# Kernel optimization log

Hardware: AMD Instinct MI355X
Metric: run time of the kernel (lower is better)

## Reference

```python
import jax, jax.numpy as jnp
import numpy as np

B, L, DIM, N, D = 8, 273, 1536, 12, 128
ZS, F_HIS = 256, 32  # image tokens per frame, cache_frame_max
EPS = 1e-6


def rmsnorm(x, g, eps=EPS):
    return x * jax.lax.rsqrt(jnp.mean(x * x, axis=-1, keepdims=True) + eps) * g


def rope_apply(x, freqs):
    # x: [B, T, N, D]; freqs: [T, D//2] angles. Rotate consecutive pairs.
    xp = x.reshape(*x.shape[:-1], D // 2, 2)
    c = jnp.cos(freqs)[None, :, None, :]
    s = jnp.sin(freqs)[None, :, None, :]
    o1 = xp[..., 0] * c - xp[..., 1] * s
    o2 = xp[..., 0] * s + xp[..., 1] * c
    return jnp.stack([o1, o2], axis=-1).reshape(x.shape)


def setup_inputs() -> dict:
    key = jax.random.key(0)
    ks = jax.random.split(key, 10)
    rn = lambda k, shp, sc=1.0: jax.random.normal(k, shp, dtype=jnp.float32) * sc
    return {
        "x": rn(ks[0], (B, L, DIM)),
        "w_q": rn(ks[1], (DIM, DIM), 0.02), "b_q": jnp.zeros((DIM,), jnp.float32),
        "w_k": rn(ks[2], (DIM, DIM), 0.02), "b_k": jnp.zeros((DIM,), jnp.float32),
        "w_v": rn(ks[3], (DIM, DIM), 0.02), "b_v": jnp.zeros((DIM,), jnp.float32),
        "w_o": rn(ks[4], (DIM, DIM), 0.02), "b_o": jnp.zeros((DIM,), jnp.float32),
        "g_q": jnp.ones((DIM,), jnp.float32), "g_k": jnp.ones((DIM,), jnp.float32),
        "cache_k": rn(ks[5], (B, F_HIS * L, N, D)),
        "cache_v": rn(ks[6], (B, F_HIS * L, N, D)),
        "rope_table": jax.random.uniform(ks[7], (64, L, D // 2), dtype=jnp.float32) * (2.0 * np.pi),
        "read_rope_indices": jnp.arange(F_HIS, dtype=jnp.int32),
        "current_frame_idx": 20,
    }


def reference(x, w_q, b_q, w_k, b_k, w_v, b_v, w_o, b_o, g_q, g_k,
              cache_k, cache_v, rope_table, read_rope_indices, current_frame_idx):
    b, s = x.shape[:2]
    f = 1  # one new frame per step (s == L)
    # qkv projections with RMSNorm over full dim (pre head split)
    q = rmsnorm(x @ w_q.T + b_q, g_q).reshape(b, s, N, D)
    k = rmsnorm(x @ w_k.T + b_k, g_k).reshape(b, s, N, D)
    v = (x @ w_v.T + b_v).reshape(b, s, N, D)
    # KV-cache ring-buffer store at slot = frame_idx % cache_frame_max
    slot = current_frame_idx % F_HIS
    cache_k = jax.lax.dynamic_update_slice(cache_k, k, (0, slot * L, 0, 0))
    cache_v = jax.lax.dynamic_update_slice(cache_v, v, (0, slot * L, 0, 0))
    # RoPE angles: history for each cache slot, last for the current frame
    freqs_his = rope_table[read_rope_indices].reshape(F_HIS * L, D // 2)
    freqs_last = rope_table[current_frame_idx]  # [L, D//2]
    q_r = rope_apply(q, freqs_last)
    k_r = rope_apply(cache_k, freqs_his)
    # frame-major views: [b, frames, tokens_per_frame, n, d]
    q_r = q_r.reshape(b, f, L, N, D)
    k_r = k_r.reshape(b, F_HIS, L, N, D)
    v_his = cache_v.reshape(b, F_HIS, L, N, D)
    q_img, k_img, v_img = q_r[:, :, :ZS], k_r[:, :, :ZS], v_his[:, :, :ZS]
    # temporal attention per spatial (image) token, non-causal, masked to valid frames
    scale = 1.0 / jnp.sqrt(jnp.asarray(D, jnp.float32))
    scores = jnp.einsum('bfznd,bgznd->bznfg', q_img, k_img) * scale  # [b,zs,n,f,f_his]
    valid = jnp.minimum(current_frame_idx + 1, F_HIS)
    keep = jnp.arange(F_HIS) < valid
    scores = jnp.where(keep[None, None, None, None, :], scores, -1e30)
    p = jax.nn.softmax(scores, axis=-1)
    x_img = jnp.einsum('bznfg,bgznd->bfznd', p, v_img)  # [b, f, zs, n, d]
    # condition tokens bypass attention: pass through v of the current frame
    v_cond = v.reshape(b, f, L, N, D)[:, :, ZS:]
    out = jnp.concatenate([x_img, v_cond], axis=2).reshape(b, s, N * D)
    return out @ w_o.T + b_o


if __name__ == '__main__':
    o = reference(**setup_inputs())
    print(o.shape)
```

## Files before the change

### kernel.cpp

```cpp
#include <hip/hip_runtime.h>
#include <hip/hip_bf16.h>
#include <stdint.h>

typedef unsigned short u16;
typedef __attribute__((ext_vector_type(8))) short bf16x8;
typedef __attribute__((ext_vector_type(4))) float f32x4;

#define B_    8
#define L_    273
#define DIM_  1536
#define NH_   12
#define DH_   128
#define ZS_   256
#define FH_   32
#define MROWS (B_ * L_)
#define MPAD  2304
#define NQKV  4608
#define WN_   (DIM_ * DIM_)
#define WN8_  (WN_ / 8)
#define X8_   (MROWS * DIM_ / 8)
#define XT8_  (MPAD * DIM_ / 8)

#define N0_ 442368
#define N1_ 737280
#define N2_ 1032192
#define N3_ 1327104
#define N4_ 1622016
#define N5_ 1626624
#define N6_ 2150912
#define PREP_BLKS 8402

#define ATTN_ITEMS (B_ * ZS_ * 6)
#define ATTN_BLKS  (ATTN_ITEMS / 2)
#define VCOND_TOT  (B_ * (L_ - ZS_) * DIM_ / 8)
#define VCOND_BLKS ((VCOND_TOT + 255) / 256)

#define KSPLIT 768

#define OFF_XB    0ULL
#define OFF_WB    7077888ULL
#define OFF_WOB   21233664ULL
#define OFF_BQKV  25952256ULL
#define OFF_CQKV  25970688ULL
#define OFF_ATTN  47204352ULL
#define OFF_SC    54282240ULL
#define OFF_P0    0ULL
#define OFF_P1    25970688ULL

__device__ __forceinline__ u16 f2bf(float f) {
  __hip_bfloat16 h = __float2bfloat16(f);
  return *reinterpret_cast<u16*>(&h);
}
__device__ __forceinline__ float bf2f(u16 v) {
  uint32_t u = ((uint32_t)v) << 16;
  return __uint_as_float(u);
}

__device__ __forceinline__ void gload_lds16(const u16* g, u16* l) {
  __builtin_amdgcn_global_load_lds(
      (const __attribute__((address_space(1))) void*)g,
      (__attribute__((address_space(3))) void*)l,
      16, 0, 0);
}

__device__ __forceinline__ void cast8(const float* __restrict__ s, u16* __restrict__ d,
                                      int i, int nvalid) {
  uint4 o;
  if (i < nvalid) {
    const float4 a = ((const float4*)s)[i * 2];
    const float4 b = ((const float4*)s)[i * 2 + 1];
    o.x = (uint32_t)f2bf(a.x) | ((uint32_t)f2bf(a.y) << 16);
    o.y = (uint32_t)f2bf(a.z) | ((uint32_t)f2bf(a.w) << 16);
    o.z = (uint32_t)f2bf(b.x) | ((uint32_t)f2bf(b.y) << 16);
    o.w = (uint32_t)f2bf(b.z) | ((uint32_t)f2bf(b.w) << 16);
  } else {
    o = make_uint4(0, 0, 0, 0);
  }
  ((uint4*)d)[i] = o;
}

__global__ __launch_bounds__(256)
void prep_kernel(const float* __restrict__ x, const float* __restrict__ w_q,
                 const float* __restrict__ w_k, const float* __restrict__ w_v,
                 const float* __restrict__ w_o, const float* __restrict__ bq,
                 const float* __restrict__ bk, const float* __restrict__ bv,
                 const float* __restrict__ rope_tb, const int* __restrict__ rope_ix,
                 u16* __restrict__ xb, u16* __restrict__ wb, u16* __restrict__ wob,
                 float* __restrict__ bqkv, float* __restrict__ sctab) {
  const int t = blockIdx.x * 256 + threadIdx.x;
  if (t < N0_)      cast8(x,   xb,           t,       X8_);
  else if (t < N1_) cast8(w_q, wb,           t - N0_, WN8_);
  else if (t < N2_) cast8(w_k, wb + WN_,     t - N1_, WN8_);
  else if (t < N3_) cast8(w_v, wb + 2 * WN_, t - N2_, WN8_);
  else if (t < N4_) cast8(w_o, wob,          t - N3_, WN8_);
  else if (t < N5_) {
    int i = t - N4_;
    float v;
    if (i < DIM_)          v = bq[i];
    else if (i < 2 * DIM_) v = bk[i - DIM_];
    else                   v = bv[i - 2 * DIM_];
    bqkv[i] = v;
  } else {
    int u = t - N5_;
    int j = u & 63;
    int idx = u >> 6;
    int f = idx >> 8, z = idx & 255;
    int fi = rope_ix[f];
    float fr = rope_tb[((size_t)fi * L_ + z) * 64 + j];
    float sn, cn;
    __sincosf(fr, &sn, &cn);
    *(float2*)&sctab[((size_t)idx << 7) + 2 * j] = make_float2(sn, cn);
  }
}

__global__ __launch_bounds__(256)
void gemm_bt_kernel(const u16* __restrict__ A, const u16* __restrict__ Bm,
                    const float* __restrict__ bias, void* __restrict__ Cv,
                    void* __restrict__ Cv2,
                    int K, int ldc, int Mvalid, int mode, int ksplit) {
  const int tn = blockIdx.x, tm = blockIdx.y;
  const int tid = threadIdx.x;
  const int lane = tid & 63;
  const int wid = tid >> 6;
  const int wm = wid >> 1, wn = wid & 1;

  __shared__ __align__(16) u16 As[2][128 * 32];
  __shared__ __align__(16) u16 Bs[2][128 * 32];

  f32x4 acc[4][4] = {};

  const int srow = tid >> 2;
  const int scol = (tid & 3) * 8;
  const u16* Abase = A + (size_t)(tm * 128 + srow) * K + scol;
  const u16* Bbase = Bm + (size_t)(tn * 128 + srow) * K + scol;
  const size_t rstep = (size_t)64 * K;
  const int lofs = srow * 32 + scol;

  const int ko = (lane >> 4) * 8;
  const int rA = wm * 64 + (lane & 15);
  const int rB = wn * 64 + (lane & 15);

  const int k0 = blockIdx.z * ksplit;
  const int k1 = k0 + ksplit;

  gload_lds16(Abase + k0,         &As[0][lofs]);
  gload_lds16(Abase + k0 + rstep, &As[0][64 * 32 + lofs]);
  gload_lds16(Bbase + k0,         &Bs[0][lofs]);
  gload_lds16(Bbase + k0 + rstep, &Bs[0][64 * 32 + lofs]);
  __syncthreads();

  int cur = 0;
  for (int kt = k0; kt < k1; kt += 32) {
    const int nx = cur ^ 1;
    if (kt + 32 < k1) {
      gload_lds16(Abase + kt + 32,         &As[nx][lofs]);
      gload_lds16(Abase + kt + 32 + rstep, &As[nx][64 * 32 + lofs]);
      gload_lds16(Bbase + kt + 32,         &Bs[nx][lofs]);
      gload_lds16(Bbase + kt + 32 + rstep, &Bs[nx][64 * 32 + lofs]);
    }
    bf16x8 af[4], bfr[4];
#pragma unroll
    for (int f = 0; f < 4; ++f) {
      af[f]  = *(const bf16x8*)&As[cur][(rA + f * 16) * 32 + ko];
      bfr[f] = *(const bf16x8*)&Bs[cur][(rB + f * 16) * 32 + ko];
    }
#pragma unroll
    for (int fm = 0; fm < 4; ++fm)
#pragma unroll
      for (int fn = 0; fn < 4; ++fn)
        acc[fm][fn] = __builtin_amdgcn_mfma_f32_16x16x32_bf16(af[fm], bfr[fn], acc[fm][fn], 0, 0, 0);
    __syncthreads();
    cur = nx;
  }

  const int m0 = tm * 128 + wm * 64 + (lane >> 4) * 4;
  const int n0 = tn * 128 + wn * 64 + (lane & 15);
  float* Cf = (mode == 2 && blockIdx.z) ? (float*)Cv2 : (float*)Cv;
#pragma unroll
  for (int fm = 0; fm < 4; ++fm) {
#pragma unroll
    for (int fn = 0; fn < 4; ++fn) {
      const int n = n0 + fn * 16;
      const float bv = (mode == 2) ? 0.f : bias[n];
#pragma unroll
      for (int r = 0; r < 4; ++r) {
        const int m = m0 + fm * 16 + r;
        if (m < Mvalid) {
          const float val = acc[fm][fn][r] + bv;
          if (mode == 1) ((u16*)Cv)[(size_t)m * ldc + n] = f2bf(val);
          else           Cf[(size_t)m * ldc + n] = val;
        }
      }
    }
  }
}

__global__ __launch_bounds__(256)
void rmsnorm_rope_kernel(u16* __restrict__ C, const float* __restrict__ g_q,
                         const float* __restrict__ g_k, const float* __restrict__ rope_table,
                         const int* __restrict__ cf_ptr) {
  const int z = blockIdx.x % ZS_;
  const int b = blockIdx.x / ZS_;
  const int m = b * L_ + z;
  const int tid = threadIdx.x;
  const int cf = *cf_ptr;
  u16* row = C + (size_t)m * NQKV;
  __shared__ float red[4];

  for (int sec = 0; sec < 2; ++sec) {
    u16* p = row + sec * DIM_;
    const float* gw = sec ? g_k : g_q;
    float vx[3], vy[3];
    float ss = 0.f;
#pragma unroll
    for (int j = 0; j < 3; ++j) {
      int pj = tid + j * 256;
      uint32_t u = *(const uint32_t*)&p[pj * 2];
      vx[j] = bf2f((u16)(u & 0xffff));
      vy[j] = bf2f((u16)(u >> 16));
      ss += vx[j] * vx[j] + vy[j] * vy[j];
    }
#pragma unroll
    for (int o = 32; o; o >>= 1) ss += __shfl_xor(ss, o);
    if ((tid & 63) == 0) red[tid >> 6] = ss;
    __syncthreads();
    const float tot = red[0] + red[1] + red[2] + red[3];
    const float r = rsqrtf(tot * (1.f / DIM_) + 1e-6f);
#pragma unroll
    for (int j = 0; j < 3; ++j) {
      int pj = tid + j * 256;
      float y0 = vx[j] * r * gw[pj * 2];
      float y1 = vy[j] * r * gw[pj * 2 + 1];
      if (sec == 0) {
        float fr = rope_table[((size_t)cf * L_ + z) * 64 + (pj & 63)];
        float sn, cn;
        __sincosf(fr, &sn, &cn);
        float o0 = y0 * cn - y1 * sn;
        float o1 = y0 * sn + y1 * cn;
        y0 = o0; y1 = o1;
      }
      *(uint32_t*)&p[pj * 2] = (uint32_t)f2bf(y0) | ((uint32_t)f2bf(y1) << 16);
    }
    __syncthreads();
  }
}

__global__ __launch_bounds__(256)
void attention_kernel(const u16* __restrict__ Cq, const float* __restrict__ cache_k,
                      const float* __restrict__ cache_v, const float* __restrict__ sctab,
                      const int* __restrict__ cf_ptr, u16* __restrict__ attn_in) {
  if (blockIdx.x >= ATTN_BLKS) {
    int i = (blockIdx.x - ATTN_BLKS) * 256 + threadIdx.x;
    if (i < VCOND_TOT) {
      int e = i * 8;
      int col = e % DIM_;
      int r = e / DIM_;
      int b = r / (L_ - ZS_);
      int lz = r % (L_ - ZS_);
      size_t mrow = (size_t)b * L_ + ZS_ + lz;
      *(uint4*)&attn_in[mrow * DIM_ + col] = *(const uint4*)&Cq[mrow * NQKV + 2 * DIM_ + col];
    }
    return;
  }

  __shared__ float sm[2][64][6];
  const int p = threadIdx.x >> 7;
  const int wi = (threadIdx.x >> 6) & 1;
  const int lane = threadIdx.x & 63;
  const int item = blockIdx.x * 2 + p;
  const int hp = item % 6;
  const int z = (item / 6) % ZS_;
  const int b = item / (6 * ZS_);
  const int h = lane >> 5, il = lane & 31;
  const int n = hp * 2 + h;
  const int d0 = il * 4;
  const int cf = *cf_ptr;
  const int slot = cf % FH_;
  const int valid = min(cf + 1, FH_);
  const int g0 = (valid + 1) >> 1;
  const int gs = wi ? g0 : 0;
  const int ge = wi ? valid : g0;

  const size_t crow = (size_t)(b * L_ + z) * NQKV + n * DH_ + d0;
  float q0, q1, q2, q3;
  {
    ushort4 qv = *(const ushort4*)&Cq[crow];
    q0 = bf2f(qv.x); q1 = bf2f(qv.y); q2 = bf2f(qv.z); q3 = bf2f(qv.w);
  }

  float mx = -1e30f, lsum = 0.f;
  float a0 = 0.f, a1 = 0.f, a2 = 0.f, a3 = 0.f;
  for (int g = gs; g < ge; ++g) {
    const float4 sc = *(const float4*)&sctab[((size_t)(g * ZS_ + z) << 7) + d0];
    float k0, k1, k2, k3, v0, v1, v2, v3;
    if (g == slot) {
      ushort4 kv = *(const ushort4*)&Cq[crow + DIM_];
      ushort4 vv = *(const ushort4*)&Cq[crow + 2 * DIM_];
      k0 = bf2f(kv.x); k1 = bf2f(kv.y); k2 = bf2f(kv.z); k3 = bf2f(kv.w);
      v0 = bf2f(vv.x); v1 = bf2f(vv.y); v2 = bf2f(vv.z); v3 = bf2f(vv.w);
    } else {
      const size_t coff = ((((size_t)b * FH_ + g) * L_ + z) * NH_ + n) * DH_ + d0;
      const float4 kk = *(const float4*)&cache_k[coff];
      const float4 vv = *(const float4*)&cache_v[coff];
      k0 = kk.x; k1 = kk.y; k2 = kk.z; k3 = kk.w;
      v0 = vv.x; v1 = vv.y; v2 = vv.z; v3 = vv.w;
    }
    const float kr0 = k0 * sc.y - k1 * sc.x;
    const float kr1 = k0 * sc.x + k1 * sc.y;
    const float kr2 = k2 * sc.w - k3 * sc.z;
    const float kr3 = k2 * sc.z + k3 * sc.w;
    float part = q0 * kr0 + q1 * kr1 + q2 * kr2 + q3 * kr3;
#pragma unroll
    for (int o = 16; o; o >>= 1) part += __shfl_xor(part, o);
    const float score = part * 0.088388347648318447f;
    const float nm = fmaxf(mx, score);
    const float scl = __expf(mx - nm);
    const float pw = __expf(score - nm);
    lsum = lsum * scl + pw;
    a0 = a0 * scl + pw * v0;
    a1 = a1 * scl + pw * v1;
    a2 = a2 * scl + pw * v2;
    a3 = a3 * scl + pw * v3;
    mx = nm;
  }

  if (wi == 1) {
    sm[p][lane][0] = mx;  sm[p][lane][1] = lsum;
    sm[p][lane][2] = a0;  sm[p][lane][3] = a1;
    sm[p][lane][4] = a2;  sm[p][lane][5] = a3;
  }
  __syncthreads();
  if (wi == 0) {
    const float mB = sm[p][lane][0], lB = sm[p][lane][1];
    const float M = fmaxf(mx, mB);
    const float wA = __expf(mx - M), wB = __expf(mB - M);
    const float L = lsum * wA + lB * wB;
    const float inv = 1.f / L;
    const float o0 = (a0 * wA + sm[p][lane][2] * wB) * inv;
    const float o1 = (a1 * wA + sm[p][lane][3] * wB) * inv;
    const float o2 = (a2 * wA + sm[p][lane][4] * wB) * inv;
    const float o3 = (a3 * wA + sm[p][lane][5] * wB) * inv;
    uint2 o;
    o.x = (uint32_t)f2bf(o0) | ((uint32_t)f2bf(o1) << 16);
    o.y = (uint32_t)f2bf(o2) | ((uint32_t)f2bf(o3) << 16);
    *(uint2*)&attn_in[(size_t)(b * L_ + z) * DIM_ + n * DH_ + d0] = o;
  }
}

__global__ __launch_bounds__(256)
void reduce_kernel(const float* __restrict__ p0, const float* __restrict__ p1,
                   const float* __restrict__ b_o, float* __restrict__ out) {
  const int i = blockIdx.x * 256 + threadIdx.x;
  if (i >= MROWS * DIM_ / 4) return;
  const int col4 = i % (DIM_ / 4);
  const float4 a = ((const float4*)p0)[i];
  const float4 b = ((const float4*)p1)[i];
  const float4 c = ((const float4*)b_o)[col4];
  float4 o;
  o.x = a.x + b.x + c.x;
  o.y = a.y + b.y + c.y;
  o.z = a.z + b.z + c.z;
  o.w = a.w + b.w + c.w;
  ((float4*)out)[i] = o;
}

extern "C" void kernel_launch(void* const* d_in, const int* in_sizes, int n_in,
                              void* d_out, int out_size, void* d_ws, size_t ws_size,
                              hipStream_t stream) {
  const float* x       = (const float*)d_in[0];
  const float* w_q     = (const float*)d_in[1];
  const float* b_q     = (const float*)d_in[2];
  const float* w_k     = (const float*)d_in[3];
  const float* b_k     = (const float*)d_in[4];
  const float* w_v     = (const float*)d_in[5];
  const float* b_v     = (const float*)d_in[6];
  const float* w_o     = (const float*)d_in[7];
  const float* b_o     = (const float*)d_in[8];
  const float* g_q     = (const float*)d_in[9];
  const float* g_k     = (const float*)d_in[10];
  const float* cache_k = (const float*)d_in[11];
  const float* cache_v = (const float*)d_in[12];
  const float* rope_tb = (const float*)d_in[13];
  const int*   rope_ix = (const int*)d_in[14];
  const int*   cf      = (const int*)d_in[15];

  char* ws = (char*)d_ws;
  u16*   xb      = (u16*)(ws + OFF_XB);
  u16*   wb      = (u16*)(ws + OFF_WB);
  u16*   wob     = (u16*)(ws + OFF_WOB);
  float* bqkv    = (float*)(ws + OFF_BQKV);
  u16*   Cq      = (u16*)(ws + OFF_CQKV);
  u16*   attn_in = (u16*)(ws + OFF_ATTN);
  float* sctab   = (float*)(ws + OFF_SC);
  float* p0      = (float*)(ws + OFF_P0);
  float* p1      = (float*)(ws + OFF_P1);

  prep_kernel<<<PREP_BLKS, 256, 0, stream>>>(x, w_q, w_k, w_v, w_o, b_q, b_k, b_v,
                                             rope_tb, rope_ix, xb, wb, wob, bqkv, sctab);

  gemm_bt_kernel<<<dim3(NQKV / 128, MPAD / 128, 1), 256, 0, stream>>>(
      xb, wb, bqkv, Cq, nullptr, DIM_, NQKV, MPAD, 1, DIM_);

  rmsnorm_rope_kernel<<<B_ * ZS_, 256, 0, stream>>>(Cq, g_q, g_k, rope_tb, cf);

  attention_kernel<<<ATTN_BLKS + VCOND_BLKS, 256, 0, stream>>>(
      Cq, cache_k, cache_v, sctab, cf, attn_in);

  gemm_bt_kernel<<<dim3(DIM_ / 128, MPAD / 128, 2), 256, 0, stream>>>(
      attn_in, wob, nullptr, p0, p1, DIM_, DIM_, MPAD, 2, KSPLIT);

  reduce_kernel<<<(MROWS * DIM_ / 4 + 255) / 256, 256, 0, stream>>>(p0, p1, b_o, (float*)d_out);
}
```

Baseline: 224.0 us.

## Split RMSNorm into stats-only kernel, fuse scaling and q-RoPE into attention; remap GEMM tiles

The in-place RMSNorm+RoPE pass over the QKV buffer becomes a small kernel that only writes per-row inverse RMS values. The gain and query RoPE are applied inside the attention kernel, with the current-frame sin/cos precomputed as an extra row of the prep table. This removes a read-modify-write of the Q and K sections. Separately, the GEMM block index is remapped to interleave tiles across 8 groups, presumably for better cache or XCD locality.

```diff
diff --git a/kernel.cpp b/kernel.cpp
--- a/kernel.cpp
+++ b/kernel.cpp
@@ -27,8 +27,8 @@
 #define N3_ 1327104
 #define N4_ 1622016
 #define N5_ 1626624
-#define N6_ 2150912
-#define PREP_BLKS 8402
+#define N6_ 2167296
+#define PREP_BLKS 8466
 
 #define ATTN_ITEMS (B_ * ZS_ * 6)
 #define ATTN_BLKS  (ATTN_ITEMS / 2)
@@ -44,6 +44,7 @@
 #define OFF_CQKV  25970688ULL
 #define OFF_ATTN  47204352ULL
 #define OFF_SC    54282240ULL
+#define OFF_RMS   58607616ULL
 #define OFF_P0    0ULL
 #define OFF_P1    25970688ULL
 
@@ -85,6 +86,7 @@
                  const float* __restrict__ w_o, const float* __restrict__ bq,
                  const float* __restrict__ bk, const float* __restrict__ bv,
                  const float* __restrict__ rope_tb, const int* __restrict__ rope_ix,
+                 const int* __restrict__ cf_ptr,
                  u16* __restrict__ xb, u16* __restrict__ wb, u16* __restrict__ wob,
                  float* __restrict__ bqkv, float* __restrict__ sctab) {
   const int t = blockIdx.x * 256 + threadIdx.x;
@@ -100,12 +102,12 @@
     else if (i < 2 * DIM_) v = bk[i - DIM_];
     else                   v = bv[i - 2 * DIM_];
     bqkv[i] = v;
-  } else {
+  } else if (t < N6_) {
     int u = t - N5_;
     int j = u & 63;
     int idx = u >> 6;
     int f = idx >> 8, z = idx & 255;
-    int fi = rope_ix[f];
+    int fi = (f == 32) ? *cf_ptr : rope_ix[f];
     float fr = rope_tb[((size_t)fi * L_ + z) * 64 + j];
     float sn, cn;
     __sincosf(fr, &sn, &cn);
@@ -118,7 +120,11 @@
                     const float* __restrict__ bias, void* __restrict__ Cv,
                     void* __restrict__ Cv2,
                     int K, int ldc, int Mvalid, int mode, int ksplit) {
-  const int tn = blockIdx.x, tm = blockIdx.y;
+  const int nwg = gridDim.x * gridDim.y;
+  const int lin = blockIdx.y * gridDim.x + blockIdx.x;
+  const int nl = (lin & 7) * (nwg >> 3) + (lin >> 3);
+  const int tn = nl % gridDim.x, tm = nl / gridDim.x;
+
   const int tid = threadIdx.x;
   const int lane = tid & 63;
   const int wid = tid >> 6;
@@ -196,58 +202,34 @@
 }
 
 __global__ __launch_bounds__(256)
-void rmsnorm_rope_kernel(u16* __restrict__ C, const float* __restrict__ g_q,
-                         const float* __restrict__ g_k, const float* __restrict__ rope_table,
-                         const int* __restrict__ cf_ptr) {
-  const int z = blockIdx.x % ZS_;
-  const int b = blockIdx.x / ZS_;
-  const int m = b * L_ + z;
-  const int tid = threadIdx.x;
-  const int cf = *cf_ptr;
-  u16* row = C + (size_t)m * NQKV;
-  __shared__ float red[4];
-
-  for (int sec = 0; sec < 2; ++sec) {
-    u16* p = row + sec * DIM_;
-    const float* gw = sec ? g_k : g_q;
-    float vx[3], vy[3];
-    float ss = 0.f;
-#pragma unroll
-    for (int j = 0; j < 3; ++j) {
-      int pj = tid + j * 256;
-      uint32_t u = *(const uint32_t*)&p[pj * 2];
-      vx[j] = bf2f((u16)(u & 0xffff));
-      vy[j] = bf2f((u16)(u >> 16));
-      ss += vx[j] * vx[j] + vy[j] * vy[j];
-    }
-#pragma unroll
-    for (int o = 32; o; o >>= 1) ss += __shfl_xor(ss, o);
-    if ((tid & 63) == 0) red[tid >> 6] = ss;
-    __syncthreads();
-    const float tot = red[0] + red[1] + red[2] + red[3];
-    const float r = rsqrtf(tot * (1.f / DIM_) + 1e-6f);
-#pragma unroll
-    for (int j = 0; j < 3; ++j) {
-      int pj = tid + j * 256;
-      float y0 = vx[j] * r * gw[pj * 2];
-      float y1 = vy[j] * r * gw[pj * 2 + 1];
-      if (sec == 0) {
-        float fr = rope_table[((size_t)cf * L_ + z) * 64 + (pj & 63)];
-        float sn, cn;
-        __sincosf(fr, &sn, &cn);
-        float o0 = y0 * cn - y1 * sn;
-        float o1 = y0 * sn + y1 * cn;
-        y0 = o0; y1 = o1;
-      }
-      *(uint32_t*)&p[pj * 2] = (uint32_t)f2bf(y0) | ((uint32_t)f2bf(y1) << 16);
-    }
-    __syncthreads();
-  }
+void rms_kernel(const u16* __restrict__ Cq, float* __restrict__ rms) {
+  const int w = blockIdx.x * 4 + (threadIdx.x >> 6);
+  const int lane = threadIdx.x & 63;
+  const int sec = w & 1;
+  const int rid = w >> 1;
+  const int b = rid >> 8, z = rid & 255;
+  const u16* p = Cq + (size_t)(b * L_ + z) * NQKV + sec * DIM_;
+  float ss = 0.f;
+#pragma unroll
+  for (int j = 0; j < 3; ++j) {
+    bf16x8 v = *(const bf16x8*)&p[lane * 8 + j * 512];
+#pragma unroll
+    for (int e = 0; e < 8; ++e) {
+      float f = bf2f((u16)v[e]);
+      ss += f * f;
+    }
+  }
+#pragma unroll
+  for (int o = 32; o; o >>= 1) ss += __shfl_xor(ss, o);
+  if (lane == 0)
+    rms[sec * 2048 + rid] = rsqrtf(ss * (1.f / DIM_) + 1e-6f);
 }
 
 __global__ __launch_bounds__(256)
 void attention_kernel(const u16* __restrict__ Cq, const float* __restrict__ cache_k,
                       const float* __restrict__ cache_v, const float* __restrict__ sctab,
+                      const float* __restrict__ rms, const float* __restrict__ g_q,
+                      const float* __restrict__ g_k,
                       const int* __restrict__ cf_ptr, u16* __restrict__ attn_in) {
   if (blockIdx.x >= ATTN_BLKS) {
     int i = (blockIdx.x - ATTN_BLKS) * 256 + threadIdx.x;
@@ -282,10 +264,20 @@
   const int ge = wi ? valid : g0;
 
   const size_t crow = (size_t)(b * L_ + z) * NQKV + n * DH_ + d0;
+  const float rq = rms[b * ZS_ + z];
   float q0, q1, q2, q3;
   {
     ushort4 qv = *(const ushort4*)&Cq[crow];
-    q0 = bf2f(qv.x); q1 = bf2f(qv.y); q2 = bf2f(qv.z); q3 = bf2f(qv.w);
+    const float4 gq = *(const float4*)&g_q[n * DH_ + d0];
+    const float u0 = bf2f(qv.x) * rq * gq.x;
+    const float u1 = bf2f(qv.y) * rq * gq.y;
+    const float u2 = bf2f(qv.z) * rq * gq.z;
+    const float u3 = bf2f(qv.w) * rq * gq.w;
+    const float4 scq = *(const float4*)&sctab[((size_t)(32 * ZS_ + z) << 7) + d0];
+    q0 = u0 * scq.y - u1 * scq.x;
+    q1 = u0 * scq.x + u1 * scq.y;
+    q2 = u2 * scq.w - u3 * scq.z;
+    q3 = u2 * scq.z + u3 * scq.w;
   }
 
   float mx = -1e30f, lsum = 0.f;
@@ -296,7 +288,12 @@
     if (g == slot) {
       ushort4 kv = *(const ushort4*)&Cq[crow + DIM_];
       ushort4 vv = *(const ushort4*)&Cq[crow + 2 * DIM_];
-      k0 = bf2f(kv.x); k1 = bf2f(kv.y); k2 = bf2f(kv.z); k3 = bf2f(kv.w);
+      const float rk = rms[2048 + b * ZS_ + z];
+      const float4 gk = *(const float4*)&g_k[n * DH_ + d0];
+      k0 = bf2f(kv.x) * rk * gk.x;
+      k1 = bf2f(kv.y) * rk * gk.y;
+      k2 = bf2f(kv.z) * rk * gk.z;
+      k3 = bf2f(kv.w) * rk * gk.w;
       v0 = bf2f(vv.x); v1 = bf2f(vv.y); v2 = bf2f(vv.z); v3 = bf2f(vv.w);
     } else {
       const size_t coff = ((((size_t)b * FH_ + g) * L_ + z) * NH_ + n) * DH_ + d0;
@@ -392,19 +389,20 @@
   u16*   Cq      = (u16*)(ws + OFF_CQKV);
   u16*   attn_in = (u16*)(ws + OFF_ATTN);
   float* sctab   = (float*)(ws + OFF_SC);
+  float* rms     = (float*)(ws + OFF_RMS);
   float* p0      = (float*)(ws + OFF_P0);
   float* p1      = (float*)(ws + OFF_P1);
 
   prep_kernel<<<PREP_BLKS, 256, 0, stream>>>(x, w_q, w_k, w_v, w_o, b_q, b_k, b_v,
-                                             rope_tb, rope_ix, xb, wb, wob, bqkv, sctab);
+                                             rope_tb, rope_ix, cf, xb, wb, wob, bqkv, sctab);
 
   gemm_bt_kernel<<<dim3(NQKV / 128, MPAD / 128, 1), 256, 0, stream>>>(
       xb, wb, bqkv, Cq, nullptr, DIM_, NQKV, MPAD, 1, DIM_);
 
-  rmsnorm_rope_kernel<<<B_ * ZS_, 256, 0, stream>>>(Cq, g_q, g_k, rope_tb, cf);
+  rms_kernel<<<1024, 256, 0, stream>>>(Cq, rms);
 
   attention_kernel<<<ATTN_BLKS + VCOND_BLKS, 256, 0, stream>>>(
-      Cq, cache_k, cache_v, sctab, cf, attn_in);
+      Cq, cache_k, cache_v, sctab, rms, g_q, g_k, cf, attn_in);
 
   gemm_bt_kernel<<<dim3(DIM_ / 128, MPAD / 128, 2), 256, 0, stream>>>(
       attn_in, wob, nullptr, p0, p1, DIM_, DIM_, MPAD, 2, KSPLIT);
```

Measured after the change: 221.9 us. No clear change (-0.9%).
